# Kernel optimization log

Hardware: AMD Instinct MI355X
Metric: run time of the kernel (lower is better)

The kernel has to match this reference:

```python
import jax, jax.numpy as jnp
import numpy as np

N_USER = 100000
N_ITEM = 150000
N = N_USER + N_ITEM
D = 64            # latdim
NNZ = 1250000     # sparse adjacency nnz
BATCH = 16384     # node_ids batch
NUM_GNN_LAYERS = 2
GD = 16           # gate_dim (mamba d_model)
DSTATE = 8
DCONV = 4
EXPAND = 2
DINNER = GD * EXPAND  # 32
DTRANK = 1            # ceil(GD/16)
TEMP = 0.8            # gate_temp


def setup_inputs() -> dict:
    key = jax.random.key(0)
    ks = jax.random.split(key, 20)
    f32 = jnp.float32
    inp = {}
    inp["user_embedding"] = jax.random.normal(ks[0], (N_USER, D), f32) * 0.02
    inp["item_embedding"] = jax.random.normal(ks[1], (N_ITEM, D), f32) * 0.02
    inp["edge_row"] = jax.random.randint(ks[2], (NNZ,), 0, N, dtype=jnp.int32)
    inp["edge_col"] = jax.random.randint(ks[3], (NNZ,), 0, N, dtype=jnp.int32)
    inp["edge_val"] = jax.random.uniform(ks[4], (NNZ,), f32) * 0.1
    inp["node_ids"] = jax.random.randint(ks[5], (BATCH,), 0, N, dtype=jnp.int32)
    # gate params (torch Linear weight layout: [out, in])
    inp["down_w"] = jax.random.normal(ks[6], (GD, D), f32) * 0.02
    inp["in_proj_w"] = jax.random.normal(ks[7], (2 * DINNER, GD), f32) * 0.05
    inp["conv_w"] = jax.random.normal(ks[8], (DINNER, DCONV), f32) * 0.1
    inp["conv_b"] = jnp.zeros((DINNER,), f32)
    inp["x_proj_w"] = jax.random.normal(ks[9], (DTRANK + 2 * DSTATE, DINNER), f32) * 0.05
    inp["dt_proj_w"] = jax.random.normal(ks[10], (DINNER, DTRANK), f32) * 0.1
    inp["dt_proj_b"] = jax.random.normal(ks[11], (DINNER,), f32) * 0.1
    inp["A_log"] = jnp.log(jnp.broadcast_to(jnp.arange(1, DSTATE + 1, dtype=f32), (DINNER, DSTATE)))
    inp["D_param"] = jnp.ones((DINNER,), f32)
    inp["out_proj_w"] = jax.random.normal(ks[12], (GD, DINNER), f32) * 0.05
    inp["ln_g"] = jnp.ones((GD,), f32)
    inp["ln_b"] = jnp.zeros((GD,), f32)
    inp["to_logit_w"] = jax.random.normal(ks[13], (1, GD), f32) * 0.02
    inp["to_logit_b"] = jnp.zeros((1,), f32)
    return inp


def _mamba(g, in_proj_w, conv_w, conv_b, x_proj_w, dt_proj_w, dt_proj_b, A_log, D_param, out_proj_w):
    # g: [B, L, GD] -- standard Mamba block (selective scan)
    Bsz, L, _ = g.shape
    xz = g @ in_proj_w.T                     # [B,L,2*DINNER]
    x, z = jnp.split(xz, 2, axis=-1)         # each [B,L,DINNER]
    # causal depthwise conv1d along L (padding = DCONV-1, truncated to L)
    xp = jnp.pad(x, ((0, 0), (DCONV - 1, 0), (0, 0)))
    xconv = sum(xp[:, k:k + L, :] * conv_w[:, k] for k in range(DCONV)) + conv_b
    x = jax.nn.silu(xconv)
    dbc = x @ x_proj_w.T                     # [B,L,DTRANK+2*DSTATE]
    dt = dbc[..., :DTRANK]
    Bm = dbc[..., DTRANK:DTRANK + DSTATE]
    Cm = dbc[..., DTRANK + DSTATE:]
    dt = jax.nn.softplus(dt @ dt_proj_w.T + dt_proj_b)   # [B,L,DINNER]
    A = -jnp.exp(A_log)                                   # [DINNER,DSTATE]
    dA = jnp.exp(dt[..., None] * A)                       # [B,L,DINNER,DSTATE]
    dBx = dt[..., None] * Bm[:, :, None, :] * x[..., None]

    def step(h, ins):
        dA_t, dBx_t = ins
        h = dA_t * h + dBx_t
        return h, h

    h0 = jnp.zeros((Bsz, DINNER, DSTATE), x.dtype)
    _, hs = jax.lax.scan(step, h0, (jnp.swapaxes(dA, 0, 1), jnp.swapaxes(dBx, 0, 1)))
    hs = jnp.swapaxes(hs, 0, 1)                           # [B,L,DINNER,DSTATE]
    y = jnp.einsum('blds,bls->bld', hs, Cm) + D_param * x
    y = y * jax.nn.silu(z)
    return y @ out_proj_w.T                               # [B,L,GD]


def reference(user_embedding, item_embedding, edge_val, down_w, in_proj_w, conv_w,
              conv_b, x_proj_w, dt_proj_w, dt_proj_b, A_log, D_param, out_proj_w,
              ln_g, ln_b, to_logit_w, to_logit_b, edge_row, edge_col, node_ids):
    embeds = jnp.concatenate([user_embedding, item_embedding], axis=0)   # [N,D]
    seqs = [embeds[node_ids]]
    for _ in range(NUM_GNN_LAYERS):
        # sparse adjacency aggregation: out[r] += val * embeds[c]
        msg = edge_val[:, None] * embeds[edge_col]                       # [NNZ,D]
        embeds = jax.ops.segment_sum(msg, edge_row, num_segments=N)      # [N,D]
        # F.normalize(p=2, dim=1)
        nrm = jnp.linalg.norm(embeds, axis=1, keepdims=True)
        embeds = embeds / jnp.maximum(nrm, 1e-12)
        seqs.append(embeds[node_ids])
    seq = jnp.stack(seqs, axis=1)                                        # [B,L,D]

    # MambaDepthGating._compute_logits (deg_cond disabled)
    g = seq @ down_w.T                                                   # [B,L,GD]
    y = _mamba(g, in_proj_w, conv_w, conv_b, x_proj_w, dt_proj_w, dt_proj_b,
               A_log, D_param, out_proj_w)
    y = y + g
    mu = y.mean(-1, keepdims=True)
    var = y.var(-1, keepdims=True)
    y = (y - mu) / jnp.sqrt(var + 1e-12) * ln_g + ln_b                   # LN eps=1e-12
    logits = (y @ to_logit_w.T + to_logit_b)[..., 0]                     # [B,L]

    # fuse_from_logits, L=3 > 2 -> softmax path, perturbed=False
    w = jax.nn.softmax(logits / max(TEMP, 1e-6), axis=1)                 # [B,L]
    fused = jnp.sum(seq * w[..., None], axis=1)                          # [B,D]
    return fused
```

## Files before the change

kernel.cpp:

```cpp
#include <hip/hip_runtime.h>
#include <math.h>

#define N_USER 100000
#define N_ITEM 150000
#define NTOT   250000
#define D64    64
#define NNZ    1250000
#define BATCH  16384
#define GD     16
#define DSTATE 8
#define DCONV  4
#define DINNER 32
#define LSEQ   3
#define NBLK1  ((NTOT + 1023) >> 10)

__global__ void zero4_kernel(int4* __restrict__ p, int n4) {
    int i = blockIdx.x * blockDim.x + threadIdx.x;
    if (i < n4) p[i] = make_int4(0, 0, 0, 0);
}

__global__ void mark_nids_kernel(const int* __restrict__ nids,
                                 unsigned char* __restrict__ nidf,
                                 unsigned char* __restrict__ needf) {
    int b = blockIdx.x * 256 + threadIdx.x;
    if (b < BATCH) { int r = nids[b]; nidf[r] = 1; needf[r] = 1; }
}

__global__ void mark_need_kernel(const int* __restrict__ erow,
                                 const int* __restrict__ ecol,
                                 const unsigned char* __restrict__ nidf,
                                 unsigned char* __restrict__ needf) {
    int e = blockIdx.x * 256 + threadIdx.x;
    if (e < NNZ && nidf[erow[e]]) needf[ecol[e]] = 1;
}

__global__ void hist_slot_kernel(const int* __restrict__ erow,
                                 const unsigned char* __restrict__ needf,
                                 int* __restrict__ cnt, int* __restrict__ slot) {
    int e = blockIdx.x * 256 + threadIdx.x;
    if (e >= NNZ) return;
    int r = erow[e];
    if (needf[r]) slot[e] = atomicAdd(&cnt[r], 1);
}

__global__ __launch_bounds__(256) void scan1_kernel(const int* __restrict__ cnt,
                                                    int* __restrict__ offs,
                                                    int* __restrict__ bsum) {
    __shared__ int lds[256];
    int t = threadIdx.x;
    int base = (blockIdx.x << 10) + (t << 2);
    int d0 = (base + 0 < NTOT) ? cnt[base + 0] : 0;
    int d1 = (base + 1 < NTOT) ? cnt[base + 1] : 0;
    int d2 = (base + 2 < NTOT) ? cnt[base + 2] : 0;
    int d3 = (base + 3 < NTOT) ? cnt[base + 3] : 0;
    int s = d0 + d1 + d2 + d3;
    lds[t] = s;
    __syncthreads();
    for (int off = 1; off < 256; off <<= 1) {
        int v = (t >= off) ? lds[t - off] : 0;
        __syncthreads();
        lds[t] += v;
        __syncthreads();
    }
    int excl = lds[t] - s;
    if (base + 0 < NTOT) offs[base + 0] = excl;
    if (base + 1 < NTOT) offs[base + 1] = excl + d0;
    if (base + 2 < NTOT) offs[base + 2] = excl + d0 + d1;
    if (base + 3 < NTOT) offs[base + 3] = excl + d0 + d1 + d2;
    if (t == 255) bsum[blockIdx.x] = lds[255];
}

__global__ __launch_bounds__(256) void scan2_kernel(int* __restrict__ bsum) {
    __shared__ int lds[256];
    int t = threadIdx.x;
    int v0 = (t < NBLK1) ? bsum[t] : 0;
    lds[t] = v0;
    __syncthreads();
    for (int off = 1; off < 256; off <<= 1) {
        int v = (t >= off) ? lds[t - off] : 0;
        __syncthreads();
        lds[t] += v;
        __syncthreads();
    }
    if (t < NBLK1) bsum[t] = lds[t] - v0;
}

__global__ void scan3_kernel(int* __restrict__ offs, const int* __restrict__ bsum,
                             const int* __restrict__ cnt) {
    int i = blockIdx.x * 256 + threadIdx.x;
    if (i >= NTOT) return;
    int v = offs[i] + bsum[i >> 10];
    offs[i] = v;
    if (i == NTOT - 1) offs[NTOT] = v + cnt[i];
}

__global__ void fill_kernel(const int* __restrict__ erow, const int* __restrict__ ecol,
                            const float* __restrict__ eval_, const int* __restrict__ offs,
                            const int* __restrict__ slot,
                            const unsigned char* __restrict__ needf,
                            int2* __restrict__ colval) {
    int e = blockIdx.x * 256 + threadIdx.x;
    if (e >= NNZ) return;
    int r = erow[e];
    if (!needf[r]) return;
    colval[offs[r] + slot[e]] = make_int2(ecol[e], __float_as_int(eval_[e]));
}

__global__ __launch_bounds__(256) void layer1_kernel(const float* __restrict__ user,
                                                     const float* __restrict__ item,
                                                     const unsigned char* __restrict__ needf,
                                                     const int*  __restrict__ offs,
                                                     const int2* __restrict__ colval,
                                                     float* __restrict__ dst) {
    const float4* user4 = (const float4*)user;
    const float4* item4 = (const float4*)item;

    int row    = (blockIdx.x << 4) + (threadIdx.x >> 4);
    int lane16 = threadIdx.x & 15;
    if (row >= NTOT) return;
    if (!needf[row]) return;
    int o0 = offs[row], o1 = offs[row + 1];

    float4 acc = make_float4(0.f, 0.f, 0.f, 0.f);
    int i = o0;
    for (; i + 2 <= o1; i += 2) {
        int2 cv0 = colval[i];
        int2 cv1 = colval[i + 1];
        const float4* s0 = (cv0.x < N_USER) ? user4 + (size_t)cv0.x * 16
                                            : item4 + (size_t)(cv0.x - N_USER) * 16;
        const float4* s1 = (cv1.x < N_USER) ? user4 + (size_t)cv1.x * 16
                                            : item4 + (size_t)(cv1.x - N_USER) * 16;
        float4 v0 = s0[lane16];
        float4 v1 = s1[lane16];
        float w0 = __int_as_float(cv0.y);
        float w1 = __int_as_float(cv1.y);
        acc.x = fmaf(w1, v1.x, fmaf(w0, v0.x, acc.x));
        acc.y = fmaf(w1, v1.y, fmaf(w0, v0.y, acc.y));
        acc.z = fmaf(w1, v1.z, fmaf(w0, v0.z, acc.z));
        acc.w = fmaf(w1, v1.w, fmaf(w0, v0.w, acc.w));
    }
    if (i < o1) {
        int2 cv = colval[i];
        const float4* s0 = (cv.x < N_USER) ? user4 + (size_t)cv.x * 16
                                           : item4 + (size_t)(cv.x - N_USER) * 16;
        float4 v = s0[lane16];
        float w = __int_as_float(cv.y);
        acc.x = fmaf(w, v.x, acc.x);
        acc.y = fmaf(w, v.y, acc.y);
        acc.z = fmaf(w, v.z, acc.z);
        acc.w = fmaf(w, v.w, acc.w);
    }

    float s = fmaf(acc.x, acc.x, fmaf(acc.y, acc.y, fmaf(acc.z, acc.z, acc.w * acc.w)));
    #pragma unroll
    for (int m = 8; m >= 1; m >>= 1) s += __shfl_xor(s, m, 64);
    float scale = 1.f / fmaxf(sqrtf(s), 1e-12f);
    float4 r;
    r.x = acc.x * scale; r.y = acc.y * scale; r.z = acc.z * scale; r.w = acc.w * scale;
    ((float4*)dst)[(size_t)row * 16 + lane16] = r;
}

__global__ __launch_bounds__(256) void layer2_kernel(const float* __restrict__ embA,
                                                     const int*  __restrict__ nids,
                                                     const int*  __restrict__ offs,
                                                     const int2* __restrict__ colval,
                                                     float* __restrict__ embBc) {
    const float4* src4 = (const float4*)embA;
    int idx    = (blockIdx.x << 4) + (threadIdx.x >> 4);
    int lane16 = threadIdx.x & 15;
    if (idx >= BATCH) return;
    int row = nids[idx];
    int o0 = offs[row], o1 = offs[row + 1];

    float4 acc = make_float4(0.f, 0.f, 0.f, 0.f);
    int i = o0;
    for (; i + 2 <= o1; i += 2) {
        int2 cv0 = colval[i];
        int2 cv1 = colval[i + 1];
        float4 v0 = src4[(size_t)cv0.x * 16 + lane16];
        float4 v1 = src4[(size_t)cv1.x * 16 + lane16];
        float w0 = __int_as_float(cv0.y);
        float w1 = __int_as_float(cv1.y);
        acc.x = fmaf(w1, v1.x, fmaf(w0, v0.x, acc.x));
        acc.y = fmaf(w1, v1.y, fmaf(w0, v0.y, acc.y));
        acc.z = fmaf(w1, v1.z, fmaf(w0, v0.z, acc.z));
        acc.w = fmaf(w1, v1.w, fmaf(w0, v0.w, acc.w));
    }
    if (i < o1) {
        int2 cv = colval[i];
        float4 v = src4[(size_t)cv.x * 16 + lane16];
        float w = __int_as_float(cv.y);
        acc.x = fmaf(w, v.x, acc.x);
        acc.y = fmaf(w, v.y, acc.y);
        acc.z = fmaf(w, v.z, acc.z);
        acc.w = fmaf(w, v.w, acc.w);
    }

    float s = fmaf(acc.x, acc.x, fmaf(acc.y, acc.y, fmaf(acc.z, acc.z, acc.w * acc.w)));
    #pragma unroll
    for (int m = 8; m >= 1; m >>= 1) s += __shfl_xor(s, m, 64);
    float scale = 1.f / fmaxf(sqrtf(s), 1e-12f);
    float4 r;
    r.x = acc.x * scale; r.y = acc.y * scale; r.z = acc.z * scale; r.w = acc.w * scale;
    ((float4*)embBc)[(size_t)idx * 16 + lane16] = r;
}

__global__ __launch_bounds__(256) void final_kernel(
    const int*   __restrict__ nids,
    const float* __restrict__ user,      const float* __restrict__ item,
    const float* __restrict__ embA,      const float* __restrict__ embBc,
    const float* __restrict__ down_w,    const float* __restrict__ in_proj_w,
    const float* __restrict__ conv_w,    const float* __restrict__ conv_b,
    const float* __restrict__ x_proj_w,  const float* __restrict__ dt_proj_w,
    const float* __restrict__ dt_proj_b, const float* __restrict__ A_log,
    const float* __restrict__ D_param,   const float* __restrict__ out_proj_w,
    const float* __restrict__ ln_g,      const float* __restrict__ ln_b,
    const float* __restrict__ to_logit_w,const float* __restrict__ to_logit_b,
    float* __restrict__ out) {

    __shared__ float4 s_rows4[16 * 49];
    __shared__ float  s_downT[D64 * GD];
    __shared__ float  s_ipxT[GD * DINNER];
    __shared__ float  s_ipzT[GD * DINNER];
    __shared__ float  s_xpT[DINNER * 17];
    __shared__ float  s_opT[DINNER * GD];
    __shared__ float  s_AT[DSTATE * DINNER];
    __shared__ float4 s_cw4[DINNER];
    __shared__ float  s_cb[DINNER], s_dtw[DINNER], s_dtb[DINNER], s_Dp[DINNER];
    __shared__ float  s_lng[GD], s_lnb[GD], s_lw[GD];
    __shared__ float  s_lb;
    __shared__ float  s_g[16 * 49];
    __shared__ float  s_xs[16 * 98];
    __shared__ float  s_dbc[16 * 49];

    int t = threadIdx.x;

    for (int i = t; i < D64 * GD; i += 256) {
        int j = i & 15, d = i >> 4;
        s_downT[i] = down_w[j * D64 + d];
    }
    for (int i = t; i < GD * DINNER; i += 256) {
        int d = i & 31, j = i >> 5;
        s_ipxT[i] = in_proj_w[d * GD + j];
        s_ipzT[i] = in_proj_w[(d + DINNER) * GD + j];
    }
    for (int i = t; i < DINNER * 17; i += 256) {
        int d = i / 17, r = i % 17;
        s_xpT[i] = x_proj_w[r * DINNER + d];
    }
    for (int i = t; i < DINNER * GD; i += 256) {
        int j = i & 15, d = i >> 4;
        s_opT[i] = out_proj_w[j * DINNER + d];
    }
    for (int i = t; i < DSTATE * DINNER; i += 256) {
        int d = i & 31, s = i >> 5;
        s_AT[i] = -expf(A_log[d * DSTATE + s]);
    }
    if (t < DINNER) {
        s_cw4[t] = ((const float4*)conv_w)[t];
        s_cb[t] = conv_b[t]; s_dtw[t] = dt_proj_w[t];
        s_dtb[t] = dt_proj_b[t]; s_Dp[t] = D_param[t];
    }
    if (t < GD) { s_lng[t] = ln_g[t]; s_lnb[t] = ln_b[t]; s_lw[t] = to_logit_w[t]; }
    if (t == 0) s_lb = to_logit_b[0];

    int wave = t >> 6, lane = t & 63;
    int grp = lane >> 4, lane16 = lane & 15;
    int eb = wave * 4 + grp;
    int b  = blockIdx.x * 16 + eb;
    {
        int nid = nids[b];
        const float4* p0 = (const float4*)((nid < N_USER) ? user + (size_t)nid * D64
                                                          : item + (size_t)(nid - N_USER) * D64);
        const float4* p1 = (const float4*)(embA + (size_t)nid * D64);
        const float4* p2 = (const float4*)(embBc + (size_t)b * D64);
        s_rows4[eb * 49 + 0 * 16 + lane16] = p0[lane16];
        s_rows4[eb * 49 + 1 * 16 + lane16] = p1[lane16];
        s_rows4[eb * 49 + 2 * 16 + lane16] = p2[lane16];
    }
    __syncthreads();

    const float* rows = (const float*)s_rows4 + eb * 196;

    {
        float a0 = 0.f, a1 = 0.f, a2 = 0.f;
        #pragma unroll
        for (int d = 0; d < D64; ++d) {
            float w = s_downT[d * GD + lane16];
            a0 = fmaf(rows[d], w, a0);
            a1 = fmaf(rows[64 + d], w, a1);
            a2 = fmaf(rows[128 + d], w, a2);
        }
        s_g[eb * 49 + 0 * GD + lane16] = a0;
        s_g[eb * 49 + 1 * GD + lane16] = a1;
        s_g[eb * 49 + 2 * GD + lane16] = a2;
    }
    __syncthreads();

    const float* ge = s_g + eb * 49;

    float xsr[2][LSEQ];
    #pragma unroll
    for (int c = 0; c < 2; ++c) {
        int d = lane16 + 16 * c;
        float xl0 = 0.f, xl1 = 0.f, xl2 = 0.f;
        #pragma unroll
        for (int j = 0; j < GD; ++j) {
            float w = s_ipxT[j * DINNER + d];
            xl0 = fmaf(ge[j], w, xl0);
            xl1 = fmaf(ge[GD + j], w, xl1);
            xl2 = fmaf(ge[2 * GD + j], w, xl2);
        }
        float4 cw = s_cw4[d]; float cb = s_cb[d];
        float a0 = fmaf(xl0, cw.w, cb);
        float a1 = fmaf(xl1, cw.w, fmaf(xl0, cw.z, cb));
        float a2 = fmaf(xl2, cw.w, fmaf(xl1, cw.z, fmaf(xl0, cw.y, cb)));
        xsr[c][0] = a0 / (1.f + __expf(-a0));
        xsr[c][1] = a1 / (1.f + __expf(-a1));
        xsr[c][2] = a2 / (1.f + __expf(-a2));
        #pragma unroll
        for (int l = 0; l < LSEQ; ++l) s_xs[eb * 98 + l * DINNER + d] = xsr[c][l];
    }
    __syncthreads();

    {
        const float* xse = s_xs + eb * 98;
        int nr = (lane16 == 0) ? 2 : 1;
        for (int it = 0; it < nr; ++it) {
            int r = (it == 0) ? lane16 : 16;
            float a0 = 0.f, a1 = 0.f, a2 = 0.f;
            #pragma unroll
            for (int d = 0; d < DINNER; ++d) {
                float w = s_xpT[d * 17 + r];
                a0 = fmaf(xse[d], w, a0);
                a1 = fmaf(xse[DINNER + d], w, a1);
                a2 = fmaf(xse[2 * DINNER + d], w, a2);
            }
            s_dbc[eb * 49 + 0 * 17 + r] = a0;
            s_dbc[eb * 49 + 1 * 17 + r] = a1;
            s_dbc[eb * 49 + 2 * 17 + r] = a2;
        }
    }
    __syncthreads();

    {
        const float* dbce = s_dbc + eb * 49;
        float h[2][DSTATE];
        #pragma unroll
        for (int c = 0; c < 2; ++c)
            #pragma unroll
            for (int s = 0; s < DSTATE; ++s) h[c][s] = 0.f;
        #pragma unroll
        for (int l = 0; l < LSEQ; ++l) {
            float dtr = dbce[l * 17];
            float Bm[DSTATE], Cm[DSTATE];
            #pragma unroll
            for (int s = 0; s < DSTATE; ++s) {
                Bm[s] = dbce[l * 17 + 1 + s];
                Cm[s] = dbce[l * 17 + 9 + s];
            }
            #pragma unroll
            for (int c = 0; c < 2; ++c) {
                int d = lane16 + 16 * c;
                float pre = fmaf(dtr, s_dtw[d], s_dtb[d]);
                float dt  = (pre > 20.f) ? pre : __logf(1.f + __expf(pre));
                float xv  = xsr[c][l];
                float dtx = dt * xv;
                float acc = 0.f;
                #pragma unroll
                for (int s = 0; s < DSTATE; ++s) {
                    float dA = __expf(dt * s_AT[s * DINNER + d]);
                    h[c][s] = fmaf(dA, h[c][s], dtx * Bm[s]);
                    acc = fmaf(h[c][s], Cm[s], acc);
                }
                float y = fmaf(s_Dp[d], xv, acc);
                float zv = 0.f;
                #pragma unroll
                for (int j = 0; j < GD; ++j)
                    zv = fmaf(ge[l * GD + j], s_ipzT[j * DINNER + d], zv);
                float ys = y * (zv / (1.f + __expf(-zv)));
                s_xs[eb * 98 + l * DINNER + d] = ys;
            }
        }
    }
    __syncthreads();

    float lg[LSEQ];
    {
        const float* yse = s_xs + eb * 98;
        #pragma unroll
        for (int l = 0; l < LSEQ; ++l) {
            float a = 0.f;
            #pragma unroll
            for (int d = 0; d < DINNER; ++d)
                a = fmaf(yse[l * DINNER + d], s_opT[d * GD + lane16], a);
            float v = a + ge[l * GD + lane16];
            float sm = v, sq = v * v;
            #pragma unroll
            for (int m = 1; m <= 8; m <<= 1) {
                sm += __shfl_xor(sm, m, 64);
                sq += __shfl_xor(sq, m, 64);
            }
            float mu  = sm * (1.f / GD);
            float var = fmaxf(sq * (1.f / GD) - mu * mu, 0.f);
            float inv = rsqrtf(var + 1e-12f);
            float lo = fmaf(fmaf((v - mu) * inv, s_lng[lane16], s_lnb[lane16]),
                            s_lw[lane16], 0.f);
            #pragma unroll
            for (int m = 1; m <= 8; m <<= 1) lo += __shfl_xor(lo, m, 64);
            lg[l] = (lo + s_lb) * 1.25f;
        }
    }

    {
        float mx = fmaxf(lg[0], fmaxf(lg[1], lg[2]));
        float e0 = __expf(lg[0] - mx), e1 = __expf(lg[1] - mx), e2 = __expf(lg[2] - mx);
        float inv = 1.f / (e0 + e1 + e2);
        float w0 = e0 * inv, w1 = e1 * inv, w2 = e2 * inv;
        float4 r0 = s_rows4[eb * 49 + 0 * 16 + lane16];
        float4 r1 = s_rows4[eb * 49 + 1 * 16 + lane16];
        float4 r2 = s_rows4[eb * 49 + 2 * 16 + lane16];
        float4 r;
        r.x = w0 * r0.x + w1 * r1.x + w2 * r2.x;
        r.y = w0 * r0.y + w1 * r1.y + w2 * r2.y;
        r.z = w0 * r0.z + w1 * r1.z + w2 * r2.z;
        r.w = w0 * r0.w + w1 * r1.w + w2 * r2.w;
        ((float4*)out)[(size_t)b * 16 + lane16] = r;
    }
}

extern "C" void kernel_launch(void* const* d_in, const int* in_sizes, int n_in,
                              void* d_out, int out_size, void* d_ws, size_t ws_size,
                              hipStream_t stream) {
    const float* user      = (const float*)d_in[0];
    const float* item      = (const float*)d_in[1];
    const int*   erow      = (const int*)  d_in[2];
    const int*   ecol      = (const int*)  d_in[3];
    const float* eval_     = (const float*)d_in[4];
    const int*   nids      = (const int*)  d_in[5];
    const float* down_w    = (const float*)d_in[6];
    const float* in_proj_w = (const float*)d_in[7];
    const float* conv_w    = (const float*)d_in[8];
    const float* conv_b    = (const float*)d_in[9];
    const float* x_proj_w  = (const float*)d_in[10];
    const float* dt_proj_w = (const float*)d_in[11];
    const float* dt_proj_b = (const float*)d_in[12];
    const float* A_log     = (const float*)d_in[13];
    const float* D_param   = (const float*)d_in[14];
    const float* out_projw = (const float*)d_in[15];
    const float* ln_g      = (const float*)d_in[16];
    const float* ln_b      = (const float*)d_in[17];
    const float* to_lw     = (const float*)d_in[18];
    const float* to_lb     = (const float*)d_in[19];
    float* out = (float*)d_out;

    char* base = (char*)d_ws;
    float* embA  = (float*)base;
    float* embBc = (float*)(base + 64000000);
    char* c = base + 64000000 + 4194304;
    int* cnt = (int*)c;
    unsigned char* nidf  = (unsigned char*)(c + 1000000);
    unsigned char* needf = (unsigned char*)(c + 1250000);
    c += 1500032;
    int* offs = (int*)c;  c += (size_t)(NTOT + 1) * 4 + 60;
    int* bsum = (int*)c;  c += 1024;
    int* slot = (int*)c;  c += (size_t)NNZ * 4;
    int2* colval = (int2*)c;

    zero4_kernel<<<(1500032 / 16 + 255) / 256, 256, 0, stream>>>((int4*)cnt, 1500032 / 16);
    mark_nids_kernel<<<(BATCH + 255) / 256, 256, 0, stream>>>(nids, nidf, needf);
    mark_need_kernel<<<(NNZ + 255) / 256, 256, 0, stream>>>(erow, ecol, nidf, needf);

    hist_slot_kernel<<<(NNZ + 255) / 256, 256, 0, stream>>>(erow, needf, cnt, slot);
    scan1_kernel<<<NBLK1, 256, 0, stream>>>(cnt, offs, bsum);
    scan2_kernel<<<1, 256, 0, stream>>>(bsum);
    scan3_kernel<<<(NTOT + 255) / 256, 256, 0, stream>>>(offs, bsum, cnt);
    fill_kernel<<<(NNZ + 255) / 256, 256, 0, stream>>>(erow, ecol, eval_, offs, slot, needf, colval);

    layer1_kernel<<<NTOT / 16, 256, 0, stream>>>(user, item, needf, offs, colval, embA);
    layer2_kernel<<<BATCH / 16, 256, 0, stream>>>(embA, nids, offs, colval, embBc);

    final_kernel<<<BATCH / 16, 256, 0, stream>>>(nids, user, item, embA, embBc,
                                                 down_w, in_proj_w, conv_w, conv_b,
                                                 x_proj_w, dt_proj_w, dt_proj_b, A_log,
                                                 D_param, out_projw, ln_g, ln_b, to_lw, to_lb, out);
}
```

Before: 266.2 us.

## Compact needed rows into a worklist and unroll SpMM gather loops by four

The mark kernels now build a compacted list of needed rows with an atomic counter, and needf becomes an int array so atomicExch can deduplicate entries. layer1 iterates over this worklist instead of scanning every row and early-exiting, which packs active rows densely into wavefronts. The gather loops in layer1 and layer2 are unrolled from two to four neighbours for more memory-level parallelism. The zero kernel is replaced with hipMemsetAsync. Costs are extra atomics during marking, a larger int flag array, and worklist order that no longer follows row order, which may hurt locality.

```diff
diff --git a/kernel.cpp b/kernel.cpp
--- a/kernel.cpp
+++ b/kernel.cpp
@@ -14,28 +14,34 @@
 #define LSEQ   3
 #define NBLK1  ((NTOT + 1023) >> 10)
 
-__global__ void zero4_kernel(int4* __restrict__ p, int n4) {
-    int i = blockIdx.x * blockDim.x + threadIdx.x;
-    if (i < n4) p[i] = make_int4(0, 0, 0, 0);
-}
-
 __global__ void mark_nids_kernel(const int* __restrict__ nids,
                                  unsigned char* __restrict__ nidf,
-                                 unsigned char* __restrict__ needf) {
+                                 int* __restrict__ needf,
+                                 int* __restrict__ nrows,
+                                 int* __restrict__ row_list) {
     int b = blockIdx.x * 256 + threadIdx.x;
-    if (b < BATCH) { int r = nids[b]; nidf[r] = 1; needf[r] = 1; }
+    if (b >= BATCH) return;
+    int r = nids[b];
+    nidf[r] = 1;
+    if (atomicExch(&needf[r], 1) == 0) row_list[atomicAdd(nrows, 1)] = r;
 }
 
 __global__ void mark_need_kernel(const int* __restrict__ erow,
                                  const int* __restrict__ ecol,
                                  const unsigned char* __restrict__ nidf,
-                                 unsigned char* __restrict__ needf) {
+                                 int* __restrict__ needf,
+                                 int* __restrict__ nrows,
+                                 int* __restrict__ row_list) {
     int e = blockIdx.x * 256 + threadIdx.x;
-    if (e < NNZ && nidf[erow[e]]) needf[ecol[e]] = 1;
+    if (e >= NNZ) return;
+    if (!nidf[erow[e]]) return;
+    int c = ecol[e];
+    if (needf[c]) return;
+    if (atomicExch(&needf[c], 1) == 0) row_list[atomicAdd(nrows, 1)] = c;
 }
 
 __global__ void hist_slot_kernel(const int* __restrict__ erow,
-                                 const unsigned char* __restrict__ needf,
+                                 const int* __restrict__ needf,
                                  int* __restrict__ cnt, int* __restrict__ slot) {
     int e = blockIdx.x * 256 + threadIdx.x;
     if (e >= NNZ) return;
@@ -97,7 +103,7 @@
 __global__ void fill_kernel(const int* __restrict__ erow, const int* __restrict__ ecol,
                             const float* __restrict__ eval_, const int* __restrict__ offs,
                             const int* __restrict__ slot,
-                            const unsigned char* __restrict__ needf,
+                            const int* __restrict__ needf,
                             int2* __restrict__ colval) {
     int e = blockIdx.x * 256 + threadIdx.x;
     if (e >= NNZ) return;
@@ -108,38 +114,41 @@
 
 __global__ __launch_bounds__(256) void layer1_kernel(const float* __restrict__ user,
                                                      const float* __restrict__ item,
-                                                     const unsigned char* __restrict__ needf,
+                                                     const int*  __restrict__ nrows,
+                                                     const int*  __restrict__ row_list,
                                                      const int*  __restrict__ offs,
                                                      const int2* __restrict__ colval,
                                                      float* __restrict__ dst) {
     const float4* user4 = (const float4*)user;
     const float4* item4 = (const float4*)item;
 
-    int row    = (blockIdx.x << 4) + (threadIdx.x >> 4);
+    int gid    = (blockIdx.x << 4) + (threadIdx.x >> 4);
     int lane16 = threadIdx.x & 15;
-    if (row >= NTOT) return;
-    if (!needf[row]) return;
+    if (gid >= nrows[0]) return;
+    int row = row_list[gid];
     int o0 = offs[row], o1 = offs[row + 1];
 
     float4 acc = make_float4(0.f, 0.f, 0.f, 0.f);
     int i = o0;
-    for (; i + 2 <= o1; i += 2) {
-        int2 cv0 = colval[i];
-        int2 cv1 = colval[i + 1];
+    for (; i + 4 <= o1; i += 4) {
+        int2 cv0 = colval[i], cv1 = colval[i + 1], cv2 = colval[i + 2], cv3 = colval[i + 3];
         const float4* s0 = (cv0.x < N_USER) ? user4 + (size_t)cv0.x * 16
                                             : item4 + (size_t)(cv0.x - N_USER) * 16;
         const float4* s1 = (cv1.x < N_USER) ? user4 + (size_t)cv1.x * 16
                                             : item4 + (size_t)(cv1.x - N_USER) * 16;
-        float4 v0 = s0[lane16];
-        float4 v1 = s1[lane16];
-        float w0 = __int_as_float(cv0.y);
-        float w1 = __int_as_float(cv1.y);
-        acc.x = fmaf(w1, v1.x, fmaf(w0, v0.x, acc.x));
-        acc.y = fmaf(w1, v1.y, fmaf(w0, v0.y, acc.y));
-        acc.z = fmaf(w1, v1.z, fmaf(w0, v0.z, acc.z));
-        acc.w = fmaf(w1, v1.w, fmaf(w0, v0.w, acc.w));
-    }
-    if (i < o1) {
+        const float4* s2 = (cv2.x < N_USER) ? user4 + (size_t)cv2.x * 16
+                                            : item4 + (size_t)(cv2.x - N_USER) * 16;
+        const float4* s3 = (cv3.x < N_USER) ? user4 + (size_t)cv3.x * 16
+                                            : item4 + (size_t)(cv3.x - N_USER) * 16;
+        float4 v0 = s0[lane16], v1 = s1[lane16], v2 = s2[lane16], v3 = s3[lane16];
+        float w0 = __int_as_float(cv0.y), w1 = __int_as_float(cv1.y);
+        float w2 = __int_as_float(cv2.y), w3 = __int_as_float(cv3.y);
+        acc.x = fmaf(w3, v3.x, fmaf(w2, v2.x, fmaf(w1, v1.x, fmaf(w0, v0.x, acc.x))));
+        acc.y = fmaf(w3, v3.y, fmaf(w2, v2.y, fmaf(w1, v1.y, fmaf(w0, v0.y, acc.y))));
+        acc.z = fmaf(w3, v3.z, fmaf(w2, v2.z, fmaf(w1, v1.z, fmaf(w0, v0.z, acc.z))));
+        acc.w = fmaf(w3, v3.w, fmaf(w2, v2.w, fmaf(w1, v1.w, fmaf(w0, v0.w, acc.w))));
+    }
+    for (; i < o1; ++i) {
         int2 cv = colval[i];
         const float4* s0 = (cv.x < N_USER) ? user4 + (size_t)cv.x * 16
                                            : item4 + (size_t)(cv.x - N_USER) * 16;
@@ -174,19 +183,20 @@
 
     float4 acc = make_float4(0.f, 0.f, 0.f, 0.f);
     int i = o0;
-    for (; i + 2 <= o1; i += 2) {
-        int2 cv0 = colval[i];
-        int2 cv1 = colval[i + 1];
+    for (; i + 4 <= o1; i += 4) {
+        int2 cv0 = colval[i], cv1 = colval[i + 1], cv2 = colval[i + 2], cv3 = colval[i + 3];
         float4 v0 = src4[(size_t)cv0.x * 16 + lane16];
         float4 v1 = src4[(size_t)cv1.x * 16 + lane16];
-        float w0 = __int_as_float(cv0.y);
-        float w1 = __int_as_float(cv1.y);
-        acc.x = fmaf(w1, v1.x, fmaf(w0, v0.x, acc.x));
-        acc.y = fmaf(w1, v1.y, fmaf(w0, v0.y, acc.y));
-        acc.z = fmaf(w1, v1.z, fmaf(w0, v0.z, acc.z));
-        acc.w = fmaf(w1, v1.w, fmaf(w0, v0.w, acc.w));
-    }
-    if (i < o1) {
+        float4 v2 = src4[(size_t)cv2.x * 16 + lane16];
+        float4 v3 = src4[(size_t)cv3.x * 16 + lane16];
+        float w0 = __int_as_float(cv0.y), w1 = __int_as_float(cv1.y);
+        float w2 = __int_as_float(cv2.y), w3 = __int_as_float(cv3.y);
+        acc.x = fmaf(w3, v3.x, fmaf(w2, v2.x, fmaf(w1, v1.x, fmaf(w0, v0.x, acc.x))));
+        acc.y = fmaf(w3, v3.y, fmaf(w2, v2.y, fmaf(w1, v1.y, fmaf(w0, v0.y, acc.y))));
+        acc.z = fmaf(w3, v3.z, fmaf(w2, v2.z, fmaf(w1, v1.z, fmaf(w0, v0.z, acc.z))));
+        acc.w = fmaf(w3, v3.w, fmaf(w2, v2.w, fmaf(w1, v1.w, fmaf(w0, v0.w, acc.w))));
+    }
+    for (; i < o1; ++i) {
         int2 cv = colval[i];
         float4 v = src4[(size_t)cv.x * 16 + lane16];
         float w = __int_as_float(cv.y);
@@ -458,18 +468,22 @@
     float* embA  = (float*)base;
     float* embBc = (float*)(base + 64000000);
     char* c = base + 64000000 + 4194304;
-    int* cnt = (int*)c;
-    unsigned char* nidf  = (unsigned char*)(c + 1000000);
-    unsigned char* needf = (unsigned char*)(c + 1250000);
-    c += 1500032;
+    int* cnt   = (int*)c;
+    int* needf = (int*)(c + 1000000);
+    int* nrows = (int*)(c + 2000000);
+    unsigned char* nidf = (unsigned char*)(c + 2000064);
+    size_t zbytes = 2250064;
+    c += zbytes;
+    int* row_list = (int*)c;  c += (size_t)NTOT * 4;
     int* offs = (int*)c;  c += (size_t)(NTOT + 1) * 4 + 60;
     int* bsum = (int*)c;  c += 1024;
     int* slot = (int*)c;  c += (size_t)NNZ * 4;
     int2* colval = (int2*)c;
 
-    zero4_kernel<<<(1500032 / 16 + 255) / 256, 256, 0, stream>>>((int4*)cnt, 1500032 / 16);
-    mark_nids_kernel<<<(BATCH + 255) / 256, 256, 0, stream>>>(nids, nidf, needf);
-    mark_need_kernel<<<(NNZ + 255) / 256, 256, 0, stream>>>(erow, ecol, nidf, needf);
+    hipMemsetAsync((void*)cnt, 0, zbytes, stream);
+
+    mark_nids_kernel<<<(BATCH + 255) / 256, 256, 0, stream>>>(nids, nidf, needf, nrows, row_list);
+    mark_need_kernel<<<(NNZ + 255) / 256, 256, 0, stream>>>(erow, ecol, nidf, needf, nrows, row_list);
 
     hist_slot_kernel<<<(NNZ + 255) / 256, 256, 0, stream>>>(erow, needf, cnt, slot);
     scan1_kernel<<<NBLK1, 256, 0, stream>>>(cnt, offs, bsum);
@@ -477,7 +491,7 @@
     scan3_kernel<<<(NTOT + 255) / 256, 256, 0, stream>>>(offs, bsum, cnt);
     fill_kernel<<<(NNZ + 255) / 256, 256, 0, stream>>>(erow, ecol, eval_, offs, slot, needf, colval);
 
-    layer1_kernel<<<NTOT / 16, 256, 0, stream>>>(user, item, needf, offs, colval, embA);
+    layer1_kernel<<<(NTOT + 15) / 16, 256, 0, stream>>>(user, item, nrows, row_list, offs, colval, embA);
     layer2_kernel<<<BATCH / 16, 256, 0, stream>>>(embA, nids, offs, colval, embBc);
 
     final_kernel<<<BATCH / 16, 256, 0, stream>>>(nids, user, item, embA, embBc,
```

Measured after the change: 477.2 us. 1.79x slower.
